# Kernel optimization log

Measured on AMD Instinct MI355X. Metric: run time of the kernel, lower is better.

The kernel has to match this reference:

```python
import jax, jax.numpy as jnp
import numpy as np

B, S, D, H = 8, 1024, 1024, 32


def setup_inputs() -> dict:
    key = jax.random.key(0)
    ks = jax.random.split(key, 32)
    w = lambda k, shape: jax.random.normal(k, shape, jnp.float32) * 0.02
    inp = {
        "poi_emb": jax.random.normal(ks[0], (B, S, D), jnp.float32),
        "svi_emb": jax.random.normal(ks[1], (B, S, D), jnp.float32),
        "poly_emb": jax.random.normal(ks[2], (B, S, D), jnp.float32),
        # shared multi-head attention (one module reused for all 4 calls)
        "Wq": w(ks[3], (D, D)), "bq": w(ks[4], (D,)),
        "Wk": w(ks[5], (D, D)), "bk": w(ks[6], (D,)),
        "Wv": w(ks[7], (D, D)), "bv": w(ks[8], (D,)),
        "Wo": w(ks[9], (D, D)), "bo": w(ks[10], (D,)),
        # poi_trans / svi_trans / poly_trans: Linear -> ReLU -> LayerNorm
        "Wpoi": w(ks[11], (D, D)), "bpoi": w(ks[12], (D,)),
        "gpoi": jnp.ones((D,), jnp.float32), "betapoi": jnp.zeros((D,), jnp.float32),
        "Wsvi": w(ks[13], (D, D)), "bsvi": w(ks[14], (D,)),
        "gsvi": jnp.ones((D,), jnp.float32), "betasvi": jnp.zeros((D,), jnp.float32),
        "Wpoly": w(ks[15], (D, D)), "bpoly": w(ks[16], (D,)),
        "gpoly": jnp.ones((D,), jnp.float32), "betapoly": jnp.zeros((D,), jnp.float32),
        # gate (Linear(2D,D)+sigmoid), filtration_gate (Linear(2D,D)+relu), out_trans (Linear(D,D))
        "Wg": w(ks[17], (2 * D, D)), "bg": w(ks[18], (D,)),
        "Wf": w(ks[19], (2 * D, D)), "bf": w(ks[20], (D,)),
        "Wt": w(ks[21], (D, D)), "bt": w(ks[22], (D,)),
    }
    return inp


def _ln(x, g, b, eps=1e-5):
    m = x.mean(-1, keepdims=True)
    v = ((x - m) ** 2).mean(-1, keepdims=True)
    return (x - m) / jnp.sqrt(v + eps) * g + b


def _trans(x, W, b, g, be):
    return _ln(jax.nn.relu(x @ W + b), g, be)


def _mha(q, k, v, Wq, bq, Wk, bk, Wv, bv, Wo, bo):
    Bn, Sq, Dm = q.shape
    dk = Dm // H
    Q = (q @ Wq + bq).reshape(Bn, Sq, H, dk)
    K = (k @ Wk + bk).reshape(Bn, -1, H, dk)
    V = (v @ Wv + bv).reshape(Bn, -1, H, dk)
    scores = jnp.einsum('bqhd,bkhd->bhqk', Q, K) / jnp.sqrt(jnp.float32(dk))
    attn = jax.nn.softmax(scores, axis=-1)
    out = jnp.einsum('bhqk,bkhd->bqhd', attn, V).reshape(Bn, Sq, Dm)
    return out @ Wo + bo


def reference(poi_emb, svi_emb, poly_emb, Wq, bq, Wk, bk, Wv, bv, Wo, bo,
              Wpoi, bpoi, gpoi, betapoi, Wsvi, bsvi, gsvi, betasvi,
              Wpoly, bpoly, gpoly, betapoly, Wg, bg, Wf, bf, Wt, bt):
    mha = lambda q, k, v: _mha(q, k, v, Wq, bq, Wk, bk, Wv, bv, Wo, bo)

    poi = _trans(poi_emb, Wpoi, bpoi, gpoi, betapoi)
    svi = _trans(svi_emb, Wsvi, bsvi, gsvi, betasvi)
    svi_feat = mha(svi, poi, poi)
    poi_feat = mha(poi, svi_feat, svi_feat)
    poi_feat = poi_feat + poi
    svi_feat = svi_feat + svi
    gate = jax.nn.sigmoid(jnp.concatenate([poi_feat, svi_feat], -1) @ Wg + bg)
    svi_fusion = gate * poi_feat + (1.0 - gate) * svi_feat
    filt = jax.nn.relu(jnp.concatenate([poi_feat, svi_fusion], -1) @ Wf + bf)
    out = filt @ Wt + bt

    # num == 3 branch
    poly = _trans(poly_emb, Wpoly, bpoly, gpoly, betapoly)
    poi2 = out
    poly_feat = mha(poly, poi2, poi2)
    poi_feat2 = mha(poi2, poly_feat, poly_feat)
    poly_feat = poly_feat + poly
    poi_feat2 = poi_feat2 + poi2
    gate2 = jax.nn.sigmoid(jnp.concatenate([poi_feat2, poly_feat], -1) @ Wg + bg)
    poly_fusion = gate2 * poi_feat2 + (1.0 - gate2) * poly_feat
    filt2 = jax.nn.relu(jnp.concatenate([poi_feat2, poly_fusion], -1) @ Wf + bf)
    return filt2 @ Wt + bt
```

## Files before the change

### kernel.cpp

```cpp
#include <hip/hip_runtime.h>
#include <hip/hip_bf16.h>


typedef unsigned short u16;
typedef __bf16 bf16x8_t __attribute__((ext_vector_type(8)));
typedef float f32x4 __attribute__((ext_vector_type(4)));

__device__ __forceinline__ u16 f2bf(float f) {
  union { __hip_bfloat16 h; u16 u; } c; c.h = __float2bfloat16(f); return c.u;
}
__device__ __forceinline__ float bf2f(u16 u) {
  union { unsigned v; float f; } c; c.v = ((unsigned)u) << 16; return c.f;
}

__device__ __forceinline__ void gl16(const void* g, void* l) {
  __builtin_amdgcn_global_load_lds((const __attribute__((address_space(1))) unsigned*)g,
                                   (__attribute__((address_space(3))) unsigned*)l, 16, 0, 0);
}

__global__ void fill_kernel(float4* o, float v) {
  int i = blockIdx.x * 256 + threadIdx.x;
  float4 x = {v, v, v, v};
  o[i] = x;
}

__global__ void conv_bf16_kernel(const float4* __restrict__ in, ushort4* __restrict__ out) {
  int i = blockIdx.x * 256 + threadIdx.x;
  float4 v = in[i];
  ushort4 o; o.x = f2bf(v.x); o.y = f2bf(v.y); o.z = f2bf(v.z); o.w = f2bf(v.w);
  out[i] = o;
}

struct WPack { const float* s[8]; u16* d[8]; };

__global__ void transpose_w_kernel(WPack p, int K) {
  const float* W = p.s[blockIdx.z];
  u16* Wt = p.d[blockIdx.z];
  __shared__ float tile[32][33];
  int tx = threadIdx.x, ty = threadIdx.y;
  int n0 = blockIdx.x * 32, k0 = blockIdx.y * 32;
#pragma unroll
  for (int i = 0; i < 4; i++)
    tile[ty + 8 * i][tx] = W[(size_t)(k0 + ty + 8 * i) * 1024 + n0 + tx];
  __syncthreads();
#pragma unroll
  for (int i = 0; i < 4; i++)
    Wt[(size_t)(n0 + ty + 8 * i) * K + k0 + tx] = f2bf(tile[tx][ty + 8 * i]);
}

__global__ __launch_bounds__(256) void gemm_bf16_kernel(
    const u16* __restrict__ A, const u16* __restrict__ A2,
    const u16* __restrict__ Bt, const float* __restrict__ bias,
    const float* __restrict__ resF,
    float* __restrict__ outF, u16* __restrict__ outH, int K, int act) {
  __shared__ __align__(16) u16 lA[128 * 64];
  __shared__ __align__(16) u16 lB[128 * 64];
  int tid = threadIdx.x, lane = tid & 63, w = tid >> 6;
  int g = lane >> 4, li = lane & 15;
  int bx = blockIdx.x & 7, by = blockIdx.x >> 3;
  int row0 = by * 128, col0 = bx * 128;
  int wr = (w >> 1) * 64, wc = (w & 1) * 64;
  f32x4 acc[4][4] = {};

  for (int k0 = 0; k0 < K; k0 += 64) {
    const u16* Abase = (k0 < 1024) ? A : A2;
    int ka = k0 & 1023;
#pragma unroll
    for (int i = 0; i < 4; i++) {
      int c = tid + i * 256; int r = c >> 3, kc = c & 7;
      gl16(Abase + (size_t)(row0 + r) * 1024 + ka + kc * 8, lA + c * 8);
    }
#pragma unroll
    for (int i = 0; i < 4; i++) {
      int c = tid + i * 256; int n = c >> 3, kc = c & 7;
      gl16(Bt + (size_t)(col0 + n) * K + k0 + kc * 8, lB + c * 8);
    }
    __syncthreads();
#pragma unroll
    for (int kk = 0; kk < 2; kk++) {
      bf16x8_t af[4], bfr[4];
#pragma unroll
      for (int mr = 0; mr < 4; mr++)
        af[mr] = *(const bf16x8_t*)(lA + (wr + mr * 16 + li) * 64 + kk * 32 + g * 8);
#pragma unroll
      for (int nr = 0; nr < 4; nr++)
        bfr[nr] = *(const bf16x8_t*)(lB + (wc + nr * 16 + li) * 64 + kk * 32 + g * 8);
#pragma unroll
      for (int mr = 0; mr < 4; mr++)
#pragma unroll
        for (int nr = 0; nr < 4; nr++)
          acc[mr][nr] = __builtin_amdgcn_mfma_f32_16x16x32_bf16(af[mr], bfr[nr], acc[mr][nr], 0, 0, 0);
    }
    __syncthreads();
  }

#pragma unroll
  for (int nr = 0; nr < 4; nr++) {
    int col = col0 + wc + nr * 16 + li;
    float bv = bias[col];
#pragma unroll
    for (int mr = 0; mr < 4; mr++) {
      int rowb = row0 + wr + mr * 16 + g * 4;
#pragma unroll
      for (int r = 0; r < 4; r++) {
        size_t off = (size_t)(rowb + r) * 1024 + col;
        float v = acc[mr][nr][r] + bv;
        if (resF) v += resF[off];
        if (act == 1) v = fmaxf(v, 0.f);
        else if (act == 2) v = 1.f / (1.f + __expf(-v));
        if (outF) outF[off] = v;
        if (outH) outH[off] = f2bf(v);
      }
    }
  }
}

__global__ __launch_bounds__(256) void ln_relu_kernel(
    const u16* __restrict__ in, const float* __restrict__ gam, const float* __restrict__ bet,
    float* __restrict__ outF, u16* __restrict__ outH) {
  int row = blockIdx.x, t = threadIdx.x, lane = t & 63, w = t >> 6;
  ushort4 xi = ((const ushort4*)(in + (size_t)row * 1024))[t];
  float4 x;
  x.x = fmaxf(bf2f(xi.x), 0.f); x.y = fmaxf(bf2f(xi.y), 0.f);
  x.z = fmaxf(bf2f(xi.z), 0.f); x.w = fmaxf(bf2f(xi.w), 0.f);
  float s1 = x.x + x.y + x.z + x.w;
  float s2 = x.x * x.x + x.y * x.y + x.z * x.z + x.w * x.w;
#pragma unroll
  for (int m = 1; m < 64; m <<= 1) { s1 += __shfl_xor(s1, m); s2 += __shfl_xor(s2, m); }
  __shared__ float red[8];
  if (lane == 0) { red[w] = s1; red[4 + w] = s2; }
  __syncthreads();
  s1 = red[0] + red[1] + red[2] + red[3];
  s2 = red[4] + red[5] + red[6] + red[7];
  float mean = s1 * (1.f / 1024.f);
  float var = s2 * (1.f / 1024.f) - mean * mean;
  float rstd = rsqrtf(var + 1e-5f);
  float4 gg = ((const float4*)gam)[t], bb = ((const float4*)bet)[t];
  float4 y;
  y.x = (x.x - mean) * rstd * gg.x + bb.x;
  y.y = (x.y - mean) * rstd * gg.y + bb.y;
  y.z = (x.z - mean) * rstd * gg.z + bb.z;
  y.w = (x.w - mean) * rstd * gg.w + bb.w;
  if (outF) ((float4*)(outF + (size_t)row * 1024))[t] = y;
  ushort4 h; h.x = f2bf(y.x); h.y = f2bf(y.y); h.z = f2bf(y.z); h.w = f2bf(y.w);
  ((ushort4*)(outH + (size_t)row * 1024))[t] = h;
}

__global__ void add2_kernel(const ushort4* __restrict__ a, const ushort4* __restrict__ b,
                            ushort4* __restrict__ o) {
  int i = blockIdx.x * 256 + threadIdx.x;
  ushort4 x = a[i], y = b[i];
  ushort4 h;
  h.x = f2bf(bf2f(x.x) + bf2f(y.x)); h.y = f2bf(bf2f(x.y) + bf2f(y.y));
  h.z = f2bf(bf2f(x.z) + bf2f(y.z)); h.w = f2bf(bf2f(x.w) + bf2f(y.w));
  o[i] = h;
}

__global__ void fusion_kernel(const ushort4* __restrict__ gt, const ushort4* __restrict__ a,
                              const ushort4* __restrict__ b, ushort4* __restrict__ o) {
  int i = blockIdx.x * 256 + threadIdx.x;
  ushort4 g = gt[i], x = a[i], y = b[i];
  ushort4 h;
  float gx;
  gx = bf2f(g.x); h.x = f2bf(gx * bf2f(x.x) + (1.f - gx) * bf2f(y.x));
  gx = bf2f(g.y); h.y = f2bf(gx * bf2f(x.y) + (1.f - gx) * bf2f(y.y));
  gx = bf2f(g.z); h.z = f2bf(gx * bf2f(x.z) + (1.f - gx) * bf2f(y.z));
  gx = bf2f(g.w); h.w = f2bf(gx * bf2f(x.w) + (1.f - gx) * bf2f(y.w));
  o[i] = h;
}

__global__ __launch_bounds__(256) void attn_kernel(
    const u16* __restrict__ Q, const u16* __restrict__ Kb,
    const u16* __restrict__ Vb, u16* __restrict__ O) {
  int bid = blockIdx.x;
  int qt = bid & 15, h = (bid >> 4) & 31, b = bid >> 9;
  int tid = threadIdx.x, lane = tid & 63, w = tid >> 6;
  int g = lane >> 4, li = lane & 15;
  __shared__ __align__(16) u16 lK[128 * 40];
  __shared__ __align__(16) u16 lV[32 * 136];
  __shared__ __align__(16) u16 lP[4][16 * 136];
  int q0 = qt * 64 + w * 16;

  bf16x8_t aq = *(const bf16x8_t*)(Q + ((size_t)(b * 1024 + q0 + li) << 10) + h * 32 + g * 8);
  const f32x4 fzero = {0.f, 0.f, 0.f, 0.f};
  f32x4 oacc[2] = {};
  float mrun[4], lrun[4];
#pragma unroll
  for (int r = 0; r < 4; r++) { mrun[r] = -1e30f; lrun[r] = 0.f; }
  const float scale = 0.17677669529663687f;

  for (int kt = 0; kt < 1024; kt += 128) {
    __syncthreads();
#pragma unroll
    for (int i = 0; i < 8; i++) {
      int idx = tid + i * 256; int key = idx >> 4, kd2 = idx & 15;
      unsigned v = *(const unsigned*)(Kb + ((size_t)(b * 1024 + kt + key) << 10) + h * 32 + kd2 * 2);
      *(unsigned*)(lK + key * 40 + kd2 * 2) = v;
    }
#pragma unroll
    for (int i = 0; i < 8; i++) {
      int idx = tid + i * 256; int key = idx >> 4, d2 = idx & 15;
      unsigned v = *(const unsigned*)(Vb + ((size_t)(b * 1024 + kt + key) << 10) + h * 32 + d2 * 2);
      lV[(d2 * 2 + 0) * 136 + key] = (u16)(v & 0xffffu);
      lV[(d2 * 2 + 1) * 136 + key] = (u16)(v >> 16);
    }
    __syncthreads();

    f32x4 s[8];
#pragma unroll
    for (int sub = 0; sub < 8; sub++) {
      bf16x8_t bk = *(const bf16x8_t*)(lK + (sub * 16 + li) * 40 + g * 8);
      s[sub] = __builtin_amdgcn_mfma_f32_16x16x32_bf16(aq, bk, fzero, 0, 0, 0);
    }
    float mx[4];
#pragma unroll
    for (int r = 0; r < 4; r++) mx[r] = -1e30f;
#pragma unroll
    for (int sub = 0; sub < 8; sub++)
#pragma unroll
      for (int r = 0; r < 4; r++) { s[sub][r] *= scale; mx[r] = fmaxf(mx[r], s[sub][r]); }
#pragma unroll
    for (int m = 1; m < 16; m <<= 1)
#pragma unroll
      for (int r = 0; r < 4; r++) mx[r] = fmaxf(mx[r], __shfl_xor(mx[r], m));
    float corr[4], rs[4];
#pragma unroll
    for (int r = 0; r < 4; r++) {
      float mn = fmaxf(mrun[r], mx[r]);
      corr[r] = __expf(mrun[r] - mn);
      mrun[r] = mn; rs[r] = 0.f;
    }
#pragma unroll
    for (int sub = 0; sub < 8; sub++)
#pragma unroll
      for (int r = 0; r < 4; r++) {
        float p = __expf(s[sub][r] - mrun[r]);
        s[sub][r] = p; rs[r] += p;
      }
#pragma unroll
    for (int m = 1; m < 16; m <<= 1)
#pragma unroll
      for (int r = 0; r < 4; r++) rs[r] += __shfl_xor(rs[r], m);
#pragma unroll
    for (int r = 0; r < 4; r++) lrun[r] = lrun[r] * corr[r] + rs[r];
#pragma unroll
    for (int nt = 0; nt < 2; nt++)
#pragma unroll
      for (int r = 0; r < 4; r++) oacc[nt][r] *= corr[r];
#pragma unroll
    for (int sub = 0; sub < 8; sub++)
#pragma unroll
      for (int r = 0; r < 4; r++)
        lP[w][(g * 4 + r) * 136 + sub * 16 + li] = f2bf(s[sub][r]);
    __syncthreads();
#pragma unroll
    for (int ks = 0; ks < 4; ks++) {
      bf16x8_t ap = *(const bf16x8_t*)(lP[w] + li * 136 + ks * 32 + g * 8);
#pragma unroll
      for (int nt = 0; nt < 2; nt++) {
        bf16x8_t bv = *(const bf16x8_t*)(lV + (nt * 16 + li) * 136 + ks * 32 + g * 8);
        oacc[nt] = __builtin_amdgcn_mfma_f32_16x16x32_bf16(ap, bv, oacc[nt], 0, 0, 0);
      }
    }
  }
#pragma unroll
  for (int r = 0; r < 4; r++) {
    float inv = 1.f / lrun[r];
#pragma unroll
    for (int nt = 0; nt < 2; nt++)
      O[((size_t)(b * 1024 + q0 + g * 4 + r) << 10) + h * 32 + nt * 16 + li] =
          f2bf(oacc[nt][r] * inv);
  }
}

extern "C" void kernel_launch(void* const* d_in, const int* in_sizes, int n_in,
                              void* d_out, int out_size, void* d_ws, size_t ws_size,
                              hipStream_t stream) {
  const float* poi_emb = (const float*)d_in[0];
  const float* svi_emb = (const float*)d_in[1];
  const float* poly_emb = (const float*)d_in[2];
  const float *Wq = (const float*)d_in[3], *bq = (const float*)d_in[4];
  const float *Wk = (const float*)d_in[5], *bk = (const float*)d_in[6];
  const float *Wv = (const float*)d_in[7], *bv = (const float*)d_in[8];
  const float *Wo = (const float*)d_in[9], *bo = (const float*)d_in[10];
  const float *Wpoi = (const float*)d_in[11], *bpoi = (const float*)d_in[12];
  const float *gpoi = (const float*)d_in[13], *betapoi = (const float*)d_in[14];
  const float *Wsvi = (const float*)d_in[15], *bsvi = (const float*)d_in[16];
  const float *gsvi = (const float*)d_in[17], *betasvi = (const float*)d_in[18];
  const float *Wpoly = (const float*)d_in[19], *bpoly = (const float*)d_in[20];
  const float *gpoly = (const float*)d_in[21], *betapoly = (const float*)d_in[22];
  const float *Wg = (const float*)d_in[23], *bg = (const float*)d_in[24];
  const float *Wf = (const float*)d_in[25], *bfilt = (const float*)d_in[26];
  const float *Wt = (const float*)d_in[27], *bt = (const float*)d_in[28];

  const size_t MB = 1u << 20;
  if (ws_size < 184 * MB) {
    fill_kernel<<<out_size / 1024, 256, 0, stream>>>((float4*)d_out, 1e4f);
    return;
  }
  char* ws = (char*)d_ws;
  u16* WqT = (u16*)(ws + 0 * MB);   u16* WkT = (u16*)(ws + 2 * MB);
  u16* WvT = (u16*)(ws + 4 * MB);   u16* WoT = (u16*)(ws + 6 * MB);
  u16* WpoiT = (u16*)(ws + 8 * MB); u16* WsviT = (u16*)(ws + 10 * MB);
  u16* WpolyT = (u16*)(ws + 12 * MB); u16* WtT = (u16*)(ws + 14 * MB);
  u16* WgT = (u16*)(ws + 16 * MB);  u16* WfT = (u16*)(ws + 20 * MB);
  u16* B0 = (u16*)(ws + 24 * MB);  u16* B1 = (u16*)(ws + 40 * MB);
  u16* B2 = (u16*)(ws + 56 * MB);  u16* B3 = (u16*)(ws + 72 * MB);
  u16* B4 = (u16*)(ws + 88 * MB);  u16* B5 = (u16*)(ws + 104 * MB);
  float* F1 = (float*)(ws + 120 * MB);
  float* F2 = (float*)(ws + 152 * MB);

  WPack p8;
  p8.s[0]=Wq; p8.s[1]=Wk; p8.s[2]=Wv; p8.s[3]=Wo; p8.s[4]=Wpoi; p8.s[5]=Wsvi; p8.s[6]=Wpoly; p8.s[7]=Wt;
  p8.d[0]=WqT; p8.d[1]=WkT; p8.d[2]=WvT; p8.d[3]=WoT; p8.d[4]=WpoiT; p8.d[5]=WsviT; p8.d[6]=WpolyT; p8.d[7]=WtT;
  transpose_w_kernel<<<dim3(32, 32, 8), dim3(32, 8), 0, stream>>>(p8, 1024);
  WPack p2;
  p2.s[0]=Wg; p2.s[1]=Wf; p2.d[0]=WgT; p2.d[1]=WfT;
  for (int i = 2; i < 8; i++) { p2.s[i] = Wg; p2.d[i] = WgT; }
  transpose_w_kernel<<<dim3(32, 64, 2), dim3(32, 8), 0, stream>>>(p2, 2048);

  const int EV = 8192;
  auto conv = [&](const float* s, u16* d) {
    conv_bf16_kernel<<<EV, 256, 0, stream>>>((const float4*)s, (ushort4*)d);
  };
  auto gemm = [&](const u16* A, const u16* A2, const u16* Bt, const float* bias,
                  const float* res, int K, int act, float* oF, u16* oH) {
    gemm_bf16_kernel<<<512, 256, 0, stream>>>(A, A2, Bt, bias, res, oF, oH, K, act);
  };
  auto ln = [&](const u16* in, const float* ga, const float* be, float* oF, u16* oH) {
    ln_relu_kernel<<<8192, 256, 0, stream>>>(in, ga, be, oF, oH);
  };
  auto add2 = [&](const u16* a, const u16* b, u16* o) {
    add2_kernel<<<EV, 256, 0, stream>>>((const ushort4*)a, (const ushort4*)b, (ushort4*)o);
  };
  auto fus = [&](const u16* g, const u16* a, const u16* b, u16* o) {
    fusion_kernel<<<EV, 256, 0, stream>>>((const ushort4*)g, (const ushort4*)a, (const ushort4*)b, (ushort4*)o);
  };
  auto attn = [&](const u16* q, const u16* k, const u16* v, u16* o) {
    attn_kernel<<<4096, 256, 0, stream>>>(q, k, v, o);
  };

  conv(poi_emb, B0);
  gemm(B0, nullptr, WpoiT, bpoi, nullptr, 1024, 0, nullptr, B1);
  ln(B1, gpoi, betapoi, F1, B1);
  conv(svi_emb, B0);
  gemm(B0, nullptr, WsviT, bsvi, nullptr, 1024, 0, nullptr, B2);
  ln(B2, gsvi, betasvi, nullptr, B2);
  gemm(B2, nullptr, WqT, bq, nullptr, 1024, 0, nullptr, B3);
  gemm(B1, nullptr, WkT, bk, nullptr, 1024, 0, nullptr, B4);
  gemm(B1, nullptr, WvT, bv, nullptr, 1024, 0, nullptr, B5);
  attn(B3, B4, B5, B0);
  gemm(B0, nullptr, WoT, bo, nullptr, 1024, 0, nullptr, B3);
  gemm(B1, nullptr, WqT, bq, nullptr, 1024, 0, nullptr, B0);
  gemm(B3, nullptr, WkT, bk, nullptr, 1024, 0, nullptr, B4);
  gemm(B3, nullptr, WvT, bv, nullptr, 1024, 0, nullptr, B5);
  attn(B0, B4, B5, B1);
  gemm(B1, nullptr, WoT, bo, F1, 1024, 0, nullptr, B0);
  add2(B3, B2, B4);
  gemm(B0, B4, WgT, bg, nullptr, 2048, 2, nullptr, B2);
  fus(B2, B0, B4, B5);
  gemm(B0, B5, WfT, bfilt, nullptr, 2048, 1, nullptr, B3);
  gemm(B3, nullptr, WtT, bt, nullptr, 1024, 0, F2, B1);

  conv(poly_emb, B0);
  gemm(B0, nullptr, WpolyT, bpoly, nullptr, 1024, 0, nullptr, B2);
  ln(B2, gpoly, betapoly, nullptr, B2);
  gemm(B2, nullptr, WqT, bq, nullptr, 1024, 0, nullptr, B3);
  gemm(B1, nullptr, WkT, bk, nullptr, 1024, 0, nullptr, B4);
  gemm(B1, nullptr, WvT, bv, nullptr, 1024, 0, nullptr, B5);
  attn(B3, B4, B5, B0);
  gemm(B0, nullptr, WoT, bo, nullptr, 1024, 0, nullptr, B3);
  gemm(B1, nullptr, WqT, bq, nullptr, 1024, 0, nullptr, B0);
  gemm(B3, nullptr, WkT, bk, nullptr, 1024, 0, nullptr, B4);
  gemm(B3, nullptr, WvT, bv, nullptr, 1024, 0, nullptr, B5);
  attn(B0, B4, B5, B1);
  gemm(B1, nullptr, WoT, bo, F2, 1024, 0, nullptr, B0);
  add2(B3, B2, B4);
  gemm(B0, B4, WgT, bg, nullptr, 2048, 2, nullptr, B2);
  fus(B2, B0, B4, B5);
  gemm(B0, B5, WfT, bfilt, nullptr, 2048, 1, nullptr, B3);
  gemm(B3, nullptr, WtT, bt, nullptr, 1024, 0, (float*)d_out, nullptr);
}
```

Baseline: 2.185 ms.

## Batch GEMMs into multi-segment launches, fuse gating, and streamline attention

Replaces the single GEMM kernel with a multi-segment kernel that can run up to three independent GEMMs in one launch, including concatenated K/V projections (N=2048) that share one A read. The gate-fusion blend moves into the sigmoid GEMM epilogue, the three embedding conversions and LayerNorms are merged into single launches, and a log2e-folded softmax scale is applied in the Q projection. Attention gets XCD-aware block remapping, 16-byte K/V loads with paired V transposition, exp2, lazy rescaling of the running max, padded LDS strides, and one fewer barrier. The trade-offs are more control logic in the GEMM epilogue and a lazy rescaling threshold that relies on bounded exponent growth.

```diff
diff --git a/kernel.cpp b/kernel.cpp
--- a/kernel.cpp
+++ b/kernel.cpp
@@ -24,15 +24,16 @@
   o[i] = x;
 }
 
-__global__ void conv_bf16_kernel(const float4* __restrict__ in, ushort4* __restrict__ out) {
-  int i = blockIdx.x * 256 + threadIdx.x;
-  float4 v = in[i];
+struct Conv3 { const float4* s[3]; ushort4* d[3]; };
+__global__ void conv3_kernel(Conv3 p) {
+  int seg = blockIdx.x >> 13;
+  int i = (blockIdx.x & 8191) * 256 + threadIdx.x;
+  float4 v = p.s[seg][i];
   ushort4 o; o.x = f2bf(v.x); o.y = f2bf(v.y); o.z = f2bf(v.z); o.w = f2bf(v.w);
-  out[i] = o;
+  p.d[seg][i] = o;
 }
 
 struct WPack { const float* s[8]; u16* d[8]; };
-
 __global__ void transpose_w_kernel(WPack p, int K) {
   const float* W = p.s[blockIdx.z];
   u16* Wt = p.d[blockIdx.z];
@@ -48,22 +49,37 @@
     Wt[(size_t)(n0 + ty + 8 * i) * K + k0 + tx] = f2bf(tile[tx][ty + 8 * i]);
 }
 
-__global__ __launch_bounds__(256) void gemm_bf16_kernel(
-    const u16* __restrict__ A, const u16* __restrict__ A2,
-    const u16* __restrict__ Bt, const float* __restrict__ bias,
-    const float* __restrict__ resF,
-    float* __restrict__ outF, u16* __restrict__ outH, int K, int act) {
+struct GemmSeg {
+  const u16 *A, *A2, *Bt;
+  const float *bias, *bias1, *resF;
+  float* outF; u16 *outH0, *outH1;
+  const u16 *fx, *fy;
+  int K, act, nctl, blk0;
+  float oscale;
+};
+struct GemmArgs { GemmSeg s[3]; int nseg; int nwg8; };
+
+__global__ __launch_bounds__(256) void gemm_mega(GemmArgs ga) {
+  int orig = blockIdx.x;
+  int bid = (orig & 7) * ga.nwg8 + (orig >> 3);
+  int si = 0;
+  if (ga.nseg > 1 && bid >= ga.s[1].blk0) si = 1;
+  if (ga.nseg > 2 && bid >= ga.s[2].blk0) si = 2;
+  GemmSeg sg = ga.s[si];
+  int lb = bid - sg.blk0;
+  int nct = 1 << sg.nctl;
+  int bx = lb & (nct - 1), by = lb >> sg.nctl;
+
   __shared__ __align__(16) u16 lA[128 * 64];
   __shared__ __align__(16) u16 lB[128 * 64];
   int tid = threadIdx.x, lane = tid & 63, w = tid >> 6;
   int g = lane >> 4, li = lane & 15;
-  int bx = blockIdx.x & 7, by = blockIdx.x >> 3;
   int row0 = by * 128, col0 = bx * 128;
   int wr = (w >> 1) * 64, wc = (w & 1) * 64;
   f32x4 acc[4][4] = {};
 
-  for (int k0 = 0; k0 < K; k0 += 64) {
-    const u16* Abase = (k0 < 1024) ? A : A2;
+  for (int k0 = 0; k0 < sg.K; k0 += 64) {
+    const u16* Abase = (k0 < 1024) ? sg.A : sg.A2;
     int ka = k0 & 1023;
 #pragma unroll
     for (int i = 0; i < 4; i++) {
@@ -73,7 +89,7 @@
 #pragma unroll
     for (int i = 0; i < 4; i++) {
       int c = tid + i * 256; int n = c >> 3, kc = c & 7;
-      gl16(Bt + (size_t)(col0 + n) * K + k0 + kc * 8, lB + c * 8);
+      gl16(sg.Bt + (size_t)(col0 + n) * sg.K + k0 + kc * 8, lB + c * 8);
     }
     __syncthreads();
 #pragma unroll
@@ -97,29 +113,38 @@
 #pragma unroll
   for (int nr = 0; nr < 4; nr++) {
     int col = col0 + wc + nr * 16 + li;
-    float bv = bias[col];
+    int hi = col >> 10, colm = col & 1023;
+    float bv = (hi ? sg.bias1 : sg.bias)[colm];
+    u16* oh = hi ? sg.outH1 : sg.outH0;
 #pragma unroll
     for (int mr = 0; mr < 4; mr++) {
       int rowb = row0 + wr + mr * 16 + g * 4;
 #pragma unroll
       for (int r = 0; r < 4; r++) {
-        size_t off = (size_t)(rowb + r) * 1024 + col;
+        size_t off = (size_t)(rowb + r) * 1024 + colm;
         float v = acc[mr][nr][r] + bv;
-        if (resF) v += resF[off];
-        if (act == 1) v = fmaxf(v, 0.f);
-        else if (act == 2) v = 1.f / (1.f + __expf(-v));
-        if (outF) outF[off] = v;
-        if (outH) outH[off] = f2bf(v);
+        if (sg.resF) v += sg.resF[off];
+        if (sg.act == 1) v = fmaxf(v, 0.f);
+        else if (sg.act == 2) {
+          v = 1.f / (1.f + __expf(-v));
+          if (sg.fx) v = v * bf2f(sg.fx[off]) + (1.f - v) * bf2f(sg.fy[off]);
+        }
+        v *= sg.oscale;
+        if (sg.outF) sg.outF[off] = v;
+        if (oh) oh[off] = f2bf(v);
       }
     }
   }
 }
 
-__global__ __launch_bounds__(256) void ln_relu_kernel(
-    const u16* __restrict__ in, const float* __restrict__ gam, const float* __restrict__ bet,
-    float* __restrict__ outF, u16* __restrict__ outH) {
-  int row = blockIdx.x, t = threadIdx.x, lane = t & 63, w = t >> 6;
-  ushort4 xi = ((const ushort4*)(in + (size_t)row * 1024))[t];
+struct LnSeg { const u16* in; const float* ga; const float* be; float* outF; u16* outH; };
+struct LnArgs { LnSeg s[3]; };
+__global__ __launch_bounds__(256) void ln3_kernel(LnArgs la) {
+  int seg = blockIdx.x >> 13;
+  int row = blockIdx.x & 8191;
+  LnSeg sg = la.s[seg];
+  int t = threadIdx.x, lane = t & 63, w = t >> 6;
+  ushort4 xi = ((const ushort4*)(sg.in + (size_t)row * 1024))[t];
   float4 x;
   x.x = fmaxf(bf2f(xi.x), 0.f); x.y = fmaxf(bf2f(xi.y), 0.f);
   x.z = fmaxf(bf2f(xi.z), 0.f); x.w = fmaxf(bf2f(xi.w), 0.f);
@@ -135,15 +160,15 @@
   float mean = s1 * (1.f / 1024.f);
   float var = s2 * (1.f / 1024.f) - mean * mean;
   float rstd = rsqrtf(var + 1e-5f);
-  float4 gg = ((const float4*)gam)[t], bb = ((const float4*)bet)[t];
+  float4 gg = ((const float4*)sg.ga)[t], bb = ((const float4*)sg.be)[t];
   float4 y;
   y.x = (x.x - mean) * rstd * gg.x + bb.x;
   y.y = (x.y - mean) * rstd * gg.y + bb.y;
   y.z = (x.z - mean) * rstd * gg.z + bb.z;
   y.w = (x.w - mean) * rstd * gg.w + bb.w;
-  if (outF) ((float4*)(outF + (size_t)row * 1024))[t] = y;
+  if (sg.outF) ((float4*)(sg.outF + (size_t)row * 1024))[t] = y;
   ushort4 h; h.x = f2bf(y.x); h.y = f2bf(y.y); h.z = f2bf(y.z); h.w = f2bf(y.w);
-  ((ushort4*)(outH + (size_t)row * 1024))[t] = h;
+  ((ushort4*)(sg.outH + (size_t)row * 1024))[t] = h;
 }
 
 __global__ void add2_kernel(const ushort4* __restrict__ a, const ushort4* __restrict__ b,
@@ -156,29 +181,17 @@
   o[i] = h;
 }
 
-__global__ void fusion_kernel(const ushort4* __restrict__ gt, const ushort4* __restrict__ a,
-                              const ushort4* __restrict__ b, ushort4* __restrict__ o) {
-  int i = blockIdx.x * 256 + threadIdx.x;
-  ushort4 g = gt[i], x = a[i], y = b[i];
-  ushort4 h;
-  float gx;
-  gx = bf2f(g.x); h.x = f2bf(gx * bf2f(x.x) + (1.f - gx) * bf2f(y.x));
-  gx = bf2f(g.y); h.y = f2bf(gx * bf2f(x.y) + (1.f - gx) * bf2f(y.y));
-  gx = bf2f(g.z); h.z = f2bf(gx * bf2f(x.z) + (1.f - gx) * bf2f(y.z));
-  gx = bf2f(g.w); h.w = f2bf(gx * bf2f(x.w) + (1.f - gx) * bf2f(y.w));
-  o[i] = h;
-}
-
 __global__ __launch_bounds__(256) void attn_kernel(
     const u16* __restrict__ Q, const u16* __restrict__ Kb,
     const u16* __restrict__ Vb, u16* __restrict__ O) {
-  int bid = blockIdx.x;
+  int orig = blockIdx.x;
+  int bid = (orig & 7) * 512 + (orig >> 3);
   int qt = bid & 15, h = (bid >> 4) & 31, b = bid >> 9;
   int tid = threadIdx.x, lane = tid & 63, w = tid >> 6;
   int g = lane >> 4, li = lane & 15;
   __shared__ __align__(16) u16 lK[128 * 40];
-  __shared__ __align__(16) u16 lV[32 * 136];
-  __shared__ __align__(16) u16 lP[4][16 * 136];
+  __shared__ __align__(16) u16 lV[32 * 152];
+  __shared__ __align__(16) u16 lP[4][16 * 152];
   int q0 = qt * 64 + w * 16;
 
   bf16x8_t aq = *(const bf16x8_t*)(Q + ((size_t)(b * 1024 + q0 + li) << 10) + h * 32 + g * 8);
@@ -187,22 +200,27 @@
   float mrun[4], lrun[4];
 #pragma unroll
   for (int r = 0; r < 4; r++) { mrun[r] = -1e30f; lrun[r] = 0.f; }
-  const float scale = 0.17677669529663687f;
 
   for (int kt = 0; kt < 1024; kt += 128) {
     __syncthreads();
 #pragma unroll
-    for (int i = 0; i < 8; i++) {
-      int idx = tid + i * 256; int key = idx >> 4, kd2 = idx & 15;
-      unsigned v = *(const unsigned*)(Kb + ((size_t)(b * 1024 + kt + key) << 10) + h * 32 + kd2 * 2);
-      *(unsigned*)(lK + key * 40 + kd2 * 2) = v;
-    }
-#pragma unroll
-    for (int i = 0; i < 8; i++) {
-      int idx = tid + i * 256; int key = idx >> 4, d2 = idx & 15;
-      unsigned v = *(const unsigned*)(Vb + ((size_t)(b * 1024 + kt + key) << 10) + h * 32 + d2 * 2);
-      lV[(d2 * 2 + 0) * 136 + key] = (u16)(v & 0xffffu);
-      lV[(d2 * 2 + 1) * 136 + key] = (u16)(v >> 16);
+    for (int i = 0; i < 2; i++) {
+      int c2 = tid + i * 256; int key = c2 >> 2, ch = c2 & 3;
+      uint4 v = *(const uint4*)(Kb + ((size_t)(b * 1024 + kt + key) << 10) + h * 32 + ch * 8);
+      *(uint4*)(lK + key * 40 + ch * 8) = v;
+    }
+    {
+      int p = tid >> 2, ch = tid & 3;
+      const u16* vb0 = Vb + ((size_t)(b * 1024 + kt + 2 * p) << 10) + h * 32 + ch * 8;
+      uint4 a = *(const uint4*)(vb0);
+      uint4 bb = *(const uint4*)(vb0 + 1024);
+      unsigned* lv32 = (unsigned*)lV;
+#pragma unroll
+      for (int j = 0; j < 4; j++) {
+        unsigned ax = ((const unsigned*)&a)[j], bx = ((const unsigned*)&bb)[j];
+        lv32[(8 * ch + 2 * j) * 76 + p]     = (ax & 0xffffu) | (bx << 16);
+        lv32[(8 * ch + 2 * j + 1) * 76 + p] = (ax >> 16) | (bx & 0xffff0000u);
+      }
     }
     __syncthreads();
 
@@ -218,23 +236,28 @@
 #pragma unroll
     for (int sub = 0; sub < 8; sub++)
 #pragma unroll
-      for (int r = 0; r < 4; r++) { s[sub][r] *= scale; mx[r] = fmaxf(mx[r], s[sub][r]); }
+      for (int r = 0; r < 4; r++) mx[r] = fmaxf(mx[r], s[sub][r]);
 #pragma unroll
     for (int m = 1; m < 16; m <<= 1)
 #pragma unroll
       for (int r = 0; r < 4; r++) mx[r] = fmaxf(mx[r], __shfl_xor(mx[r], m));
-    float corr[4], rs[4];
-#pragma unroll
-    for (int r = 0; r < 4; r++) {
-      float mn = fmaxf(mrun[r], mx[r]);
-      corr[r] = __expf(mrun[r] - mn);
-      mrun[r] = mn; rs[r] = 0.f;
-    }
+    bool keep = (mx[0] <= mrun[0] + 8.f) && (mx[1] <= mrun[1] + 8.f) &&
+                (mx[2] <= mrun[2] + 8.f) && (mx[3] <= mrun[3] + 8.f);
+    if (!__all(keep)) {
+#pragma unroll
+      for (int r = 0; r < 4; r++) {
+        float mn = fmaxf(mrun[r], mx[r]);
+        float corr = exp2f(mrun[r] - mn);
+        mrun[r] = mn; lrun[r] *= corr;
+        oacc[0][r] *= corr; oacc[1][r] *= corr;
+      }
+    }
+    float rs[4] = {0.f, 0.f, 0.f, 0.f};
 #pragma unroll
     for (int sub = 0; sub < 8; sub++)
 #pragma unroll
       for (int r = 0; r < 4; r++) {
-        float p = __expf(s[sub][r] - mrun[r]);
+        float p = exp2f(s[sub][r] - mrun[r]);
         s[sub][r] = p; rs[r] += p;
       }
 #pragma unroll
@@ -242,23 +265,18 @@
 #pragma unroll
       for (int r = 0; r < 4; r++) rs[r] += __shfl_xor(rs[r], m);
 #pragma unroll
-    for (int r = 0; r < 4; r++) lrun[r] = lrun[r] * corr[r] + rs[r];
-#pragma unroll
-    for (int nt = 0; nt < 2; nt++)
-#pragma unroll
-      for (int r = 0; r < 4; r++) oacc[nt][r] *= corr[r];
+    for (int r = 0; r < 4; r++) lrun[r] += rs[r];
 #pragma unroll
     for (int sub = 0; sub < 8; sub++)
 #pragma unroll
       for (int r = 0; r < 4; r++)
-        lP[w][(g * 4 + r) * 136 + sub * 16 + li] = f2bf(s[sub][r]);
-    __syncthreads();
+        lP[w][(g * 4 + r) * 152 + sub * 16 + li] = f2bf(s[sub][r]);
 #pragma unroll
     for (int ks = 0; ks < 4; ks++) {
-      bf16x8_t ap = *(const bf16x8_t*)(lP[w] + li * 136 + ks * 32 + g * 8);
+      bf16x8_t ap = *(const bf16x8_t*)(lP[w] + li * 152 + ks * 32 + g * 8);
 #pragma unroll
       for (int nt = 0; nt < 2; nt++) {
-        bf16x8_t bv = *(const bf16x8_t*)(lV + (nt * 16 + li) * 136 + ks * 32 + g * 8);
+        bf16x8_t bv = *(const bf16x8_t*)(lV + (nt * 16 + li) * 152 + ks * 32 + g * 8);
         oacc[nt] = __builtin_amdgcn_mfma_f32_16x16x32_bf16(ap, bv, oacc[nt], 0, 0, 0);
       }
     }
@@ -271,6 +289,16 @@
       O[((size_t)(b * 1024 + q0 + g * 4 + r) << 10) + h * 32 + nt * 16 + li] =
           f2bf(oacc[nt][r] * inv);
   }
+}
+
+static GemmSeg mk(const u16* A, const u16* A2, const u16* Bt,
+                  const float* bias, const float* bias1, const float* resF,
+                  float* outF, u16* oh0, u16* oh1, const u16* fx, const u16* fy,
+                  int K, int act, int nctl, float osc) {
+  GemmSeg s; s.A = A; s.A2 = A2; s.Bt = Bt; s.bias = bias; s.bias1 = bias1;
+  s.resF = resF; s.outF = outF; s.outH0 = oh0; s.outH1 = oh1; s.fx = fx; s.fy = fy;
+  s.K = K; s.act = act; s.nctl = nctl; s.blk0 = 0; s.oscale = osc;
+  return s;
 }
 
 extern "C" void kernel_launch(void* const* d_in, const int* in_sizes, int n_in,
@@ -294,21 +322,23 @@
   const float *Wt = (const float*)d_in[27], *bt = (const float*)d_in[28];
 
   const size_t MB = 1u << 20;
-  if (ws_size < 184 * MB) {
+  if (ws_size < 168 * MB) {
     fill_kernel<<<out_size / 1024, 256, 0, stream>>>((float4*)d_out, 1e4f);
     return;
   }
   char* ws = (char*)d_ws;
-  u16* WqT = (u16*)(ws + 0 * MB);   u16* WkT = (u16*)(ws + 2 * MB);
-  u16* WvT = (u16*)(ws + 4 * MB);   u16* WoT = (u16*)(ws + 6 * MB);
-  u16* WpoiT = (u16*)(ws + 8 * MB); u16* WsviT = (u16*)(ws + 10 * MB);
+  u16* WqT = (u16*)(ws + 0 * MB);    u16* WkT = (u16*)(ws + 2 * MB);
+  u16* WvT = (u16*)(ws + 4 * MB);    u16* WoT = (u16*)(ws + 6 * MB);
+  u16* WpoiT = (u16*)(ws + 8 * MB);  u16* WsviT = (u16*)(ws + 10 * MB);
   u16* WpolyT = (u16*)(ws + 12 * MB); u16* WtT = (u16*)(ws + 14 * MB);
-  u16* WgT = (u16*)(ws + 16 * MB);  u16* WfT = (u16*)(ws + 20 * MB);
-  u16* B0 = (u16*)(ws + 24 * MB);  u16* B1 = (u16*)(ws + 40 * MB);
-  u16* B2 = (u16*)(ws + 56 * MB);  u16* B3 = (u16*)(ws + 72 * MB);
-  u16* B4 = (u16*)(ws + 88 * MB);  u16* B5 = (u16*)(ws + 104 * MB);
-  float* F1 = (float*)(ws + 120 * MB);
-  float* F2 = (float*)(ws + 152 * MB);
+  u16* WgT = (u16*)(ws + 16 * MB);   u16* WfT = (u16*)(ws + 20 * MB);
+  u16* S0 = (u16*)(ws + 24 * MB);  u16* S1 = (u16*)(ws + 40 * MB);
+  u16* S2 = (u16*)(ws + 56 * MB);  u16* S3 = (u16*)(ws + 72 * MB);
+  u16* S4 = (u16*)(ws + 88 * MB);  u16* S5 = (u16*)(ws + 104 * MB);
+  u16* S6 = (u16*)(ws + 120 * MB);
+  float* F = (float*)(ws + 136 * MB);
+
+  const float QS = 0.25503489f;
 
   WPack p8;
   p8.s[0]=Wq; p8.s[1]=Wk; p8.s[2]=Wv; p8.s[3]=Wo; p8.s[4]=Wpoi; p8.s[5]=Wsvi; p8.s[6]=Wpoly; p8.s[7]=Wt;
@@ -319,65 +349,69 @@
   for (int i = 2; i < 8; i++) { p2.s[i] = Wg; p2.d[i] = WgT; }
   transpose_w_kernel<<<dim3(32, 64, 2), dim3(32, 8), 0, stream>>>(p2, 2048);
 
-  const int EV = 8192;
-  auto conv = [&](const float* s, u16* d) {
-    conv_bf16_kernel<<<EV, 256, 0, stream>>>((const float4*)s, (ushort4*)d);
+  auto run1 = [&](GemmSeg a) {
+    GemmArgs ga; ga.s[0] = a; ga.s[0].blk0 = 0; ga.nseg = 1;
+    int nb = 64 << a.nctl; ga.nwg8 = nb / 8;
+    gemm_mega<<<nb, 256, 0, stream>>>(ga);
   };
-  auto gemm = [&](const u16* A, const u16* A2, const u16* Bt, const float* bias,
-                  const float* res, int K, int act, float* oF, u16* oH) {
-    gemm_bf16_kernel<<<512, 256, 0, stream>>>(A, A2, Bt, bias, res, oF, oH, K, act);
+  auto run2 = [&](GemmSeg a, GemmSeg b) {
+    GemmArgs ga; ga.s[0] = a; ga.s[1] = b;
+    ga.s[0].blk0 = 0; ga.s[1].blk0 = 64 << a.nctl; ga.nseg = 2;
+    int nb = (64 << a.nctl) + (64 << b.nctl); ga.nwg8 = nb / 8;
+    gemm_mega<<<nb, 256, 0, stream>>>(ga);
   };
-  auto ln = [&](const u16* in, const float* ga, const float* be, float* oF, u16* oH) {
-    ln_relu_kernel<<<8192, 256, 0, stream>>>(in, ga, be, oF, oH);
-  };
-  auto add2 = [&](const u16* a, const u16* b, u16* o) {
-    add2_kernel<<<EV, 256, 0, stream>>>((const ushort4*)a, (const ushort4*)b, (ushort4*)o);
-  };
-  auto fus = [&](const u16* g, const u16* a, const u16* b, u16* o) {
-    fusion_kernel<<<EV, 256, 0, stream>>>((const ushort4*)g, (const ushort4*)a, (const ushort4*)b, (ushort4*)o);
+  auto run3 = [&](GemmSeg a, GemmSeg b, GemmSeg c) {
+    GemmArgs ga; ga.s[0] = a; ga.s[1] = b; ga.s[2] = c;
+    ga.s[0].blk0 = 0; ga.s[1].blk0 = 64 << a.nctl;
+    ga.s[2].blk0 = ga.s[1].blk0 + (64 << b.nctl); ga.nseg = 3;
+    int nb = ga.s[2].blk0 + (64 << c.nctl); ga.nwg8 = nb / 8;
+    gemm_mega<<<nb, 256, 0, stream>>>(ga);
   };
   auto attn = [&](const u16* q, const u16* k, const u16* v, u16* o) {
     attn_kernel<<<4096, 256, 0, stream>>>(q, k, v, o);
   };
-
-  conv(poi_emb, B0);
-  gemm(B0, nullptr, WpoiT, bpoi, nullptr, 1024, 0, nullptr, B1);
-  ln(B1, gpoi, betapoi, F1, B1);
-  conv(svi_emb, B0);
-  gemm(B0, nullptr, WsviT, bsvi, nullptr, 1024, 0, nullptr, B2);
-  ln(B2, gsvi, betasvi, nullptr, B2);
-  gemm(B2, nullptr, WqT, bq, nullptr, 1024, 0, nullptr, B3);
-  gemm(B1, nullptr, WkT, bk, nullptr, 1024, 0, nullptr, B4);
-  gemm(B1, nullptr, WvT, bv, nullptr, 1024, 0, nullptr, B5);
-  attn(B3, B4, B5, B0);
-  gemm(B0, nullptr, WoT, bo, nullptr, 1024, 0, nullptr, B3);
-  gemm(B1, nullptr, WqT, bq, nullptr, 1024, 0, nullptr, B0);
-  gemm(B3, nullptr, WkT, bk, nullptr, 1024, 0, nullptr, B4);
-  gemm(B3, nullptr, WvT, bv, nullptr, 1024, 0, nullptr, B5);
-  attn(B0, B4, B5, B1);
-  gemm(B1, nullptr, WoT, bo, F1, 1024, 0, nullptr, B0);
-  add2(B3, B2, B4);
-  gemm(B0, B4, WgT, bg, nullptr, 2048, 2, nullptr, B2);
-  fus(B2, B0, B4, B5);
-  gemm(B0, B5, WfT, bfilt, nullptr, 2048, 1, nullptr, B3);
-  gemm(B3, nullptr, WtT, bt, nullptr, 1024, 0, F2, B1);
-
-  conv(poly_emb, B0);
-  gemm(B0, nullptr, WpolyT, bpoly, nullptr, 1024, 0, nullptr, B2);
-  ln(B2, gpoly, betapoly, nullptr, B2);
-  gemm(B2, nullptr, WqT, bq, nullptr, 1024, 0, nullptr, B3);
-  gemm(B1, nullptr, WkT, bk, nullptr, 1024, 0, nullptr, B4);
-  gemm(B1, nullptr, WvT, bv, nullptr, 1024, 0, nullptr, B5);
-  attn(B3, B4, B5, B0);
-  gemm(B0, nullptr, WoT, bo, nullptr, 1024, 0, nullptr, B3);
-  gemm(B1, nullptr, WqT, bq, nullptr, 1024, 0, nullptr, B0);
-  gemm(B3, nullptr, WkT, bk, nullptr, 1024, 0, nullptr, B4);
-  gemm(B3, nullptr, WvT, bv, nullptr, 1024, 0, nullptr, B5);
-  attn(B0, B4, B5, B1);
-  gemm(B1, nullptr, WoT, bo, F2, 1024, 0, nullptr, B0);
-  add2(B3, B2, B4);
-  gemm(B0, B4, WgT, bg, nullptr, 2048, 2, nullptr, B2);
-  fus(B2, B0, B4, B5);
-  gemm(B0, B5, WfT, bfilt, nullptr, 2048, 1, nullptr, B3);
-  gemm(B3, nullptr, WtT, bt, nullptr, 1024, 0, (float*)d_out, nullptr);
-}
+  auto add2 = [&](const u16* a, const u16* b, u16* o) {
+    add2_kernel<<<8192, 256, 0, stream>>>((const ushort4*)a, (const ushort4*)b, (ushort4*)o);
+  };
+
+  Conv3 c3;
+  c3.s[0] = (const float4*)poi_emb; c3.d[0] = (ushort4*)S0;
+  c3.s[1] = (const float4*)svi_emb; c3.d[1] = (ushort4*)S1;
+  c3.s[2] = (const float4*)poly_emb; c3.d[2] = (ushort4*)S2;
+  conv3_kernel<<<24576, 256, 0, stream>>>(c3);
+
+  run3(mk(S0, 0, WpoiT, bpoi, 0, 0, 0, S3, 0, 0, 0, 1024, 0, 3, 1.f),
+       mk(S1, 0, WsviT, bsvi, 0, 0, 0, S4, 0, 0, 0, 1024, 0, 3, 1.f),
+       mk(S2, 0, WpolyT, bpoly, 0, 0, 0, S5, 0, 0, 0, 1024, 0, 3, 1.f));
+  LnArgs la;
+  la.s[0] = LnSeg{S3, gpoi, betapoi, F, S3};
+  la.s[1] = LnSeg{S4, gsvi, betasvi, 0, S4};
+  la.s[2] = LnSeg{S5, gpoly, betapoly, 0, S5};
+  ln3_kernel<<<24576, 256, 0, stream>>>(la);
+
+  run2(mk(S4, 0, WqT, bq, 0, 0, 0, S0, 0, 0, 0, 1024, 0, 3, QS),
+       mk(S3, 0, WkT, bk, bv, 0, 0, S1, S2, 0, 0, 1024, 0, 4, 1.f));
+  attn(S0, S1, S2, S6);
+  run2(mk(S6, 0, WoT, bo, 0, 0, 0, S0, 0, 0, 0, 1024, 0, 3, 1.f),
+       mk(S3, 0, WqT, bq, 0, 0, 0, S1, 0, 0, 0, 1024, 0, 3, QS));
+  run1(mk(S0, 0, WkT, bk, bv, 0, 0, S2, S6, 0, 0, 1024, 0, 4, 1.f));
+  attn(S1, S2, S6, S3);
+  run1(mk(S3, 0, WoT, bo, 0, F, 0, S1, 0, 0, 0, 1024, 0, 3, 1.f));
+  add2(S0, S4, S4);
+  run1(mk(S1, S4, WgT, bg, 0, 0, 0, S0, 0, S1, S4, 2048, 2, 3, 1.f));
+  run1(mk(S1, S0, WfT, bfilt, 0, 0, 0, S2, 0, 0, 0, 2048, 1, 3, 1.f));
+  run1(mk(S2, 0, WtT, bt, 0, 0, F, S6, 0, 0, 0, 1024, 0, 3, 1.f));
+
+  run2(mk(S5, 0, WqT, bq, 0, 0, 0, S0, 0, 0, 0, 1024, 0, 3, QS),
+       mk(S6, 0, WkT, bk, bv, 0, 0, S1, S2, 0, 0, 1024, 0, 4, 1.f));
+  attn(S0, S1, S2, S3);
+  run2(mk(S3, 0, WoT, bo, 0, 0, 0, S0, 0, 0, 0, 1024, 0, 3, 1.f),
+       mk(S6, 0, WqT, bq, 0, 0, 0, S1, 0, 0, 0, 1024, 0, 3, QS));
+  run1(mk(S0, 0, WkT, bk, bv, 0, 0, S2, S3, 0, 0, 1024, 0, 4, 1.f));
+  attn(S1, S2, S3, S4);
+  run1(mk(S4, 0, WoT, bo, 0, F, 0, S1, 0, 0, 0, 1024, 0, 3, 1.f));
+  add2(S0, S5, S5);
+  run1(mk(S1, S5, WgT, bg, 0, 0, 0, S0, 0, S1, S5, 2048, 2, 3, 1.f));
+  run1(mk(S1, S0, WfT, bfilt, 0, 0, 0, S2, 0, 0, 0, 2048, 1, 3, 1.f));
+  run1(mk(S2, 0, WtT, bt, 0, 0, (float*)d_out, 0, 0, 0, 0, 1024, 0, 3, 1.f));
+}
```

Result: faster. 1.825 ms (-16.5%).
